# Kernel optimization log

Hardware: AMD Instinct MI355X
Metric: run time of the kernel (lower is better)

The kernel has to match this reference:

```python
import jax, jax.numpy as jnp
import numpy as np

B, N_IN, D_IN, N_OUT, D_OUT, ROUTINGS = 512, 1152, 8, 10, 16, 3


def squash(s, axis=-1):
    # scale = |s|^2 / (1 + |s|^2) / (|s| + 1e-8)
    norm = jnp.linalg.norm(s, axis=axis, keepdims=True)
    return (norm ** 2 / (1.0 + norm ** 2) / (norm + 1e-8)) * s


def setup_inputs() -> dict:
    key = jax.random.key(0)
    k1, k2 = jax.random.split(key)
    x = jax.random.normal(k1, (B, N_IN, D_IN), dtype=jnp.float32)
    weight = 0.01 * jax.random.normal(k2, (N_OUT, N_IN, D_OUT, D_IN), dtype=jnp.float32)
    return {"x": x, "weight": weight}


def reference(x, weight):
    # x: [B, N_IN, D_IN]; weight: [N_OUT, N_IN, D_OUT, D_IN]
    # x_hat[b,o,n,:] = weight[o,n] @ x[b,n]  -> [B, N_OUT, N_IN, D_OUT]
    x_hat = jnp.einsum('onij,bnj->boni', weight, x)
    x_hat_det = jax.lax.stop_gradient(x_hat)

    # routing logits b: [B, N_OUT, N_IN]
    b = jnp.zeros(x_hat.shape[:3], dtype=x_hat.dtype)
    outputs = None
    for i in range(ROUTINGS):
        c = jax.nn.softmax(b, axis=1)  # softmax over output capsules
        if i == ROUTINGS - 1:
            outputs = squash(jnp.sum(c[..., None] * x_hat, axis=2))  # [B, N_OUT, D_OUT]
        else:
            outputs = squash(jnp.sum(c[..., None] * x_hat_det, axis=2))
            # agreement: b += <outputs, x_hat_det> over D_OUT
            b = b + jnp.einsum('bod,bond->bon', outputs, x_hat_det)
    return outputs  # [B, N_OUT, D_OUT]
```

## Files before the change

### kernel.cpp

```cpp
#include <hip/hip_runtime.h>
#include <hip/hip_bf16.h>
#include <hip/hip_fp16.h>

#define B_    512
#define NI    1152
#define NO    10
#define BT    16
#define NBT   32
#define NC    24
#define NCH   48
#define RNDS  6
#define RN    8

typedef __attribute__((ext_vector_type(8))) short bf16x8;
typedef __attribute__((ext_vector_type(4))) float f32x4;
typedef __attribute__((ext_vector_type(8))) unsigned short u16x8;

#define SPART_H    ((size_t)NC * NBT * NO * 256)
#define OUTSUM_F32 ((size_t)NBT * NO * 256)
#define XB_US      ((size_t)NBT * NC * RNDS * 1024)
#define WB_US      ((size_t)NC * RNDS * 12288)

__device__ inline unsigned short f2bf(float f) {
    __hip_bfloat16 h = __float2bfloat16(f);
    return *reinterpret_cast<unsigned short*>(&h);
}

__device__ __forceinline__ bf16x8 load_cvt8(const float* src) {
    f32x4 v0 = *reinterpret_cast<const f32x4*>(src);
    f32x4 v1 = *reinterpret_cast<const f32x4*>(src + 4);
    u16x8 u = { f2bf(v0[0]), f2bf(v0[1]), f2bf(v0[2]), f2bf(v0[3]),
                f2bf(v1[0]), f2bf(v1[1]), f2bf(v1[2]), f2bf(v1[3]) };
    return *reinterpret_cast<bf16x8*>(&u);
}

__device__ __forceinline__ void iter_epilogue(
    uint2 (*red)[NO * 64], const f32x4* sacc, float sc,
    int w, int l, int tid, unsigned short* base)
{
    #pragma unroll
    for (int o = 0; o < NO; ++o) {
        __half2 h01 = __floats2half2_rn(sacc[o][0] * sc, sacc[o][1] * sc);
        __half2 h23 = __floats2half2_rn(sacc[o][2] * sc, sacc[o][3] * sc);
        red[w][o * 64 + l] =
            make_uint2(*reinterpret_cast<unsigned int*>(&h01),
                       *reinterpret_cast<unsigned int*>(&h23));
    }
    __syncthreads();
    for (int g = tid; g < NO * 64; g += 256) {
        uint2 a0 = red[0][g], a1 = red[1][g], a2 = red[2][g], a3 = red[3][g];
        auto h2f2 = [](unsigned int u) {
            __half2 h = *reinterpret_cast<__half2*>(&u);
            return __half22float2(h);
        };
        float2 lo = h2f2(a0.x), l1 = h2f2(a1.x), l2 = h2f2(a2.x), l3 = h2f2(a3.x);
        float2 ho = h2f2(a0.y), h1 = h2f2(a1.y), h2 = h2f2(a2.y), h3 = h2f2(a3.y);
        float2 sl = { (lo.x + l1.x) + (l2.x + l3.x), (lo.y + l1.y) + (l2.y + l3.y) };
        float2 sh = { (ho.x + h1.x) + (h2.x + h3.x), (ho.y + h1.y) + (h2.y + h3.y) };
        __half2 p01 = __floats2half2_rn(sl.x, sl.y);
        __half2 p23 = __floats2half2_rn(sh.x, sh.y);
        *reinterpret_cast<uint2*>(base + (size_t)g * 4) =
            make_uint2(*reinterpret_cast<unsigned int*>(&p01),
                       *reinterpret_cast<unsigned int*>(&p23));
    }
}

__global__ __launch_bounds__(256) void caps_f0(
    const float* __restrict__ x, const float* __restrict__ w,
    unsigned short* __restrict__ xb, unsigned short* __restrict__ wb,
    unsigned short* __restrict__ s_part)
{
    __shared__ uint2 red[4][NO * 64];

    const int tid = threadIdx.x;
    const int wv  = tid >> 6;
    const int l   = tid & 63;
    const int b16 = l & 15;
    const int hi  = l >> 4;
    const int blk = blockIdx.x;
    const int xcd = blk & 7, idx = blk >> 3;
    const int nc  = xcd * 3 + (idx >> 5);
    const int bt  = idx & 31;

    #pragma unroll
    for (int k = 0; k < 3; ++k) {
        const int gid = k * 256 + tid;
        const int r   = gid >> 7, m = gid & 127;
        const int nl  = m >> 4, bl = m & 15;
        const int b   = bt * BT + bl;
        const int n   = nc * NCH + r * RN + nl;
        const size_t img = (size_t)(bt * NC + nc) * RNDS + r;
        bf16x8 u = load_cvt8(x + ((size_t)b * NI + n) * 8);
        *reinterpret_cast<bf16x8*>(xb + (img * 128 + m) * 8) = u;
    }

    #pragma unroll
    for (int k = 0; k < 2; ++k) {
        const int loc = k * 256 + tid;
        if (loc < 288) {
            const int t    = blk * 288 + loc;
            const int lane = t & 63;
            const int gs   = (t >> 6) % 24;
            const int img  = t / 1536;
            const int h2   = lane >> 4, d = lane & 15;
            const int nl   = gs / 3, oq = gs % 3;
            const int r    = img % RNDS, ncw = img / RNDS;
            const int o    = oq * 4 + h2;
            const int n    = ncw * NCH + r * RN + nl;
            bf16x8 u = (bf16x8){0,0,0,0,0,0,0,0};
            if (o < NO)
                u = load_cvt8(w + ((size_t)o * NI + n) * 128 + d * 8);
            *reinterpret_cast<bf16x8*>(wb + (size_t)t * 8) = u;
        }
    }

    f32x4 sacc[NO];
    #pragma unroll
    for (int o = 0; o < NO; ++o) sacc[o] = (f32x4){0.f, 0.f, 0.f, 0.f};

    const int bg = bt * BT + b16;
    #pragma unroll 1
    for (int g = 0; g < 3; ++g) {
        const int n_lane = nc * NCH + wv * 12 + g * 4 + hi;
        bf16x8 bv4 = load_cvt8(x + ((size_t)bg * NI + n_lane) * 8);
        #pragma unroll
        for (int o = 0; o < NO; ++o) {
            bf16x8 av4 = load_cvt8(w + ((size_t)o * NI + n_lane) * 128 + b16 * 8);
            sacc[o] = __builtin_amdgcn_mfma_f32_16x16x32_bf16(
                av4, bv4, sacc[o], 0, 0, 0);
        }
    }

    iter_epilogue(red, sacc, 0.1f, wv, l, tid,
                  s_part + ((size_t)nc * NBT + bt) * 2560);
}

__global__ __launch_bounds__(256, 3) void caps_itr(
    const unsigned short* __restrict__ xb,
    const unsigned short* __restrict__ wb,
    const float* __restrict__ outsum,
    unsigned short* __restrict__ s_part)
{
    __shared__ uint2 red[4][NO * 64];

    const int tid = threadIdx.x;
    const int wv  = tid >> 6;
    const int l   = tid & 63;
    const int b16 = l & 15;
    const int hi  = l >> 4;
    const int blk = blockIdx.x;
    const int xcd = blk & 7, idx = blk >> 3;
    const int nc  = xcd * 3 + (idx >> 5);
    const int bt  = idx & 31;

    f32x4 outf[NO];
    #pragma unroll
    for (int o = 0; o < NO; ++o)
        outf[o] = *reinterpret_cast<const f32x4*>(
            outsum + (((size_t)bt * NO + o) * 64 + l) * 4);

    f32x4 sacc[NO];
    #pragma unroll
    for (int o = 0; o < NO; ++o) sacc[o] = (f32x4){0.f, 0.f, 0.f, 0.f};

    const unsigned short* xbase = xb + (size_t)(bt * NC + nc) * (RNDS * 1024);
    const unsigned short* wbase = wb + (size_t)nc * (RNDS * 12288);

    #pragma unroll 1
    for (int r = 0; r < RNDS; ++r) {
        const unsigned short* xr = xbase + (size_t)r * 1024;
        const unsigned short* wr = wbase + (size_t)r * 12288;
        #pragma unroll 1
        for (int i = 0; i < 2; ++i) {
            const int nl = wv * 2 + i;
            bf16x8 bv = *reinterpret_cast<const bf16x8*>(
                xr + nl * 128 + b16 * 8);
            bf16x8 avv[3];
            #pragma unroll
            for (int oq = 0; oq < 3; ++oq)
                avv[oq] = *reinterpret_cast<const bf16x8*>(
                    wr + (nl * 3 + oq) * 512 + l * 8);
            bf16x8 bvt[4];
            #pragma unroll
            for (int t = 0; t < 4; ++t)
                bvt[t] = (hi == t) ? bv : (bf16x8){0,0,0,0,0,0,0,0};

            f32x4 xh[NO];
            float lg[NO];
            #pragma unroll
            for (int oq = 0; oq < 3; ++oq) {
                const int tmax = (oq < 2) ? 4 : 2;
                #pragma unroll
                for (int t = 0; t < tmax; ++t) {
                    const int o = oq * 4 + t;
                    xh[o] = __builtin_amdgcn_mfma_f32_16x16x32_bf16(
                        avv[oq], bvt[t], (f32x4){0.f, 0.f, 0.f, 0.f}, 0, 0, 0);
                    float pp = outf[o][0] * xh[o][0];
                    pp = fmaf(outf[o][1], xh[o][1], pp);
                    pp = fmaf(outf[o][2], xh[o][2], pp);
                    pp = fmaf(outf[o][3], xh[o][3], pp);
                    pp += __shfl_xor(pp, 16, 64);
                    pp += __shfl_xor(pp, 32, 64);
                    lg[o] = pp;
                }
            }
            float sum = 0.f;
            #pragma unroll
            for (int o = 0; o < NO; ++o) { lg[o] = __expf(lg[o]); sum += lg[o]; }
            const float rs = __builtin_amdgcn_rcpf(sum);
            #pragma unroll
            for (int o = 0; o < NO; ++o) {
                const float cc = lg[o] * rs;
                sacc[o][0] = fmaf(cc, xh[o][0], sacc[o][0]);
                sacc[o][1] = fmaf(cc, xh[o][1], sacc[o][1]);
                sacc[o][2] = fmaf(cc, xh[o][2], sacc[o][2]);
                sacc[o][3] = fmaf(cc, xh[o][3], sacc[o][3]);
            }
        }
    }

    iter_epilogue(red, sacc, 1.0f, wv, l, tid,
                  s_part + ((size_t)nc * NBT + bt) * 2560);
}

template<int MODE>
__global__ __launch_bounds__(256) void caps_squash(
    const unsigned short* __restrict__ s_part,
    float* __restrict__ outsum,
    float* __restrict__ dout)
{
    __shared__ float sq[256];
    const int bo = blockIdx.x;
    const int t  = threadIdx.x;

    float s = 0.f;
    #pragma unroll 4
    for (int nc = 0; nc < NC; ++nc) {
        __half h = *reinterpret_cast<const __half*>(
            s_part + ((size_t)nc * NBT * NO + bo) * 256 + t);
        s += __half2float(h);
    }

    float n2 = s * s;
    n2 += __shfl_xor(n2, 1, 64);
    n2 += __shfl_xor(n2, 2, 64);
    sq[t] = n2;
    __syncthreads();
    const int base = t & 63;
    n2 = (sq[base] + sq[64 + base]) + (sq[128 + base] + sq[192 + base]);

    const float norm  = sqrtf(n2);
    const float scale = n2 / ((1.f + n2) * (norm + 1e-8f));
    const float v = scale * s;

    if constexpr (MODE == 0) {
        outsum[(size_t)bo * 256 + t] = v;
    } else if constexpr (MODE == 1) {
        outsum[(size_t)bo * 256 + t] += v;
    } else {
        const int bt = bo / NO, o = bo - bt * NO;
        const int b16 = (t >> 2) & 15, hi = t >> 6, q = t & 3;
        dout[((size_t)(bt * BT + b16) * NO + o) * 16 + hi * 4 + q] = v;
    }
}

extern "C" void kernel_launch(void* const* d_in, const int* in_sizes, int n_in,
                              void* d_out, int out_size, void* d_ws, size_t ws_size,
                              hipStream_t stream) {
    const float* x = (const float*)d_in[0];
    const float* w = (const float*)d_in[1];
    float* out = (float*)d_out;

    unsigned short* s_part = (unsigned short*)d_ws;
    float*          outsum = (float*)(s_part + SPART_H);
    unsigned short* xb     = (unsigned short*)(outsum + OUTSUM_F32);
    unsigned short* wb     = xb + XB_US;

    dim3 gI(NBT * NC), bI(256);
    dim3 gS(NBT * NO), bS(256);

    caps_f0<<<gI, bI, 0, stream>>>(x, w, xb, wb, s_part);
    caps_squash<0><<<gS, bS, 0, stream>>>(s_part, outsum, nullptr);
    caps_itr<<<gI, bI, 0, stream>>>(xb, wb, outsum, s_part);
    caps_squash<1><<<gS, bS, 0, stream>>>(s_part, outsum, nullptr);
    caps_itr<<<gI, bI, 0, stream>>>(xb, wb, outsum, s_part);
    caps_squash<2><<<gS, bS, 0, stream>>>(s_part, nullptr, out);
}
```

Measured before the change: 68.27 us.

## Fuse intermediate squash reductions into routing iteration kernel prologue

The two intermediate caps_squash launches are removed. Each caps_itr block now reduces the fp16 partial sums across all chunks itself, applies squash, and builds its agreement vectors directly. The s_part buffer is double-buffered so one iteration can read the previous partials while writing new ones. Only the first iteration writes outsum; the second adds the stored value in registers. This saves two kernel launches and their dependency gaps, but every one of the 24 chunk blocks per batch tile now repeats the same cross-chunk reduction, which adds a lot of redundant L2 traffic and serial latency before the MFMA loop starts.

Result: slower. 109.1 us (+59.8%).

```diff
diff --git a/kernel.cpp b/kernel.cpp
--- a/kernel.cpp
+++ b/kernel.cpp
@@ -135,11 +135,13 @@
                   s_part + ((size_t)nc * NBT + bt) * 2560);
 }
 
+template<int IT>
 __global__ __launch_bounds__(256, 3) void caps_itr(
     const unsigned short* __restrict__ xb,
     const unsigned short* __restrict__ wb,
-    const float* __restrict__ outsum,
-    unsigned short* __restrict__ s_part)
+    const unsigned short* __restrict__ s_prev,
+    float* __restrict__ outsum,
+    unsigned short* __restrict__ s_next)
 {
     __shared__ uint2 red[4][NO * 64];
 
@@ -155,9 +157,33 @@
 
     f32x4 outf[NO];
     #pragma unroll
-    for (int o = 0; o < NO; ++o)
-        outf[o] = *reinterpret_cast<const f32x4*>(
-            outsum + (((size_t)bt * NO + o) * 64 + l) * 4);
+    for (int o = 0; o < NO; ++o) {
+        f32x4 s = (f32x4){0.f, 0.f, 0.f, 0.f};
+        #pragma unroll 6
+        for (int c = 0; c < NC; ++c) {
+            uint2 pk = *reinterpret_cast<const uint2*>(
+                s_prev + ((((size_t)c * NBT + bt) * NO + o) * 64 + l) * 4);
+            __half2 h01 = *reinterpret_cast<__half2*>(&pk.x);
+            __half2 h23 = *reinterpret_cast<__half2*>(&pk.y);
+            float2 f01 = __half22float2(h01), f23 = __half22float2(h23);
+            s[0] += f01.x; s[1] += f01.y; s[2] += f23.x; s[3] += f23.y;
+        }
+        float n2 = s[0] * s[0] + s[1] * s[1] + s[2] * s[2] + s[3] * s[3];
+        n2 += __shfl_xor(n2, 16, 64);
+        n2 += __shfl_xor(n2, 32, 64);
+        const float norm  = sqrtf(n2);
+        const float scale = n2 / ((1.f + n2) * (norm + 1e-8f));
+        f32x4 v = { scale * s[0], scale * s[1], scale * s[2], scale * s[3] };
+        if constexpr (IT == 1) {
+            *reinterpret_cast<f32x4*>(
+                outsum + (((size_t)bt * NO + o) * 64 + l) * 4) = v;
+            outf[o] = v;
+        } else {
+            f32x4 p = *reinterpret_cast<const f32x4*>(
+                outsum + (((size_t)bt * NO + o) * 64 + l) * 4);
+            outf[o] = (f32x4){p[0] + v[0], p[1] + v[1], p[2] + v[2], p[3] + v[3]};
+        }
+    }
 
     f32x4 sacc[NO];
     #pragma unroll
@@ -220,13 +246,11 @@
     }
 
     iter_epilogue(red, sacc, 1.0f, wv, l, tid,
-                  s_part + ((size_t)nc * NBT + bt) * 2560);
-}
-
-template<int MODE>
-__global__ __launch_bounds__(256) void caps_squash(
+                  s_next + ((size_t)nc * NBT + bt) * 2560);
+}
+
+__global__ __launch_bounds__(256) void caps_squash_final(
     const unsigned short* __restrict__ s_part,
-    float* __restrict__ outsum,
     float* __restrict__ dout)
 {
     __shared__ float sq[256];
@@ -253,15 +277,9 @@
     const float scale = n2 / ((1.f + n2) * (norm + 1e-8f));
     const float v = scale * s;
 
-    if constexpr (MODE == 0) {
-        outsum[(size_t)bo * 256 + t] = v;
-    } else if constexpr (MODE == 1) {
-        outsum[(size_t)bo * 256 + t] += v;
-    } else {
-        const int bt = bo / NO, o = bo - bt * NO;
-        const int b16 = (t >> 2) & 15, hi = t >> 6, q = t & 3;
-        dout[((size_t)(bt * BT + b16) * NO + o) * 16 + hi * 4 + q] = v;
-    }
+    const int bt = bo / NO, o = bo - bt * NO;
+    const int b16 = (t >> 2) & 15, hi = t >> 6, q = t & 3;
+    dout[((size_t)(bt * BT + b16) * NO + o) * 16 + hi * 4 + q] = v;
 }
 
 extern "C" void kernel_launch(void* const* d_in, const int* in_sizes, int n_in,
@@ -271,18 +289,17 @@
     const float* w = (const float*)d_in[1];
     float* out = (float*)d_out;
 
-    unsigned short* s_part = (unsigned short*)d_ws;
-    float*          outsum = (float*)(s_part + SPART_H);
-    unsigned short* xb     = (unsigned short*)(outsum + OUTSUM_F32);
-    unsigned short* wb     = xb + XB_US;
+    unsigned short* s_partA = (unsigned short*)d_ws;
+    unsigned short* s_partB = s_partA + SPART_H;
+    float*          outsum  = (float*)(s_partB + SPART_H);
+    unsigned short* xb      = (unsigned short*)(outsum + OUTSUM_F32);
+    unsigned short* wb      = xb + XB_US;
 
     dim3 gI(NBT * NC), bI(256);
     dim3 gS(NBT * NO), bS(256);
 
-    caps_f0<<<gI, bI, 0, stream>>>(x, w, xb, wb, s_part);
-    caps_squash<0><<<gS, bS, 0, stream>>>(s_part, outsum, nullptr);
-    caps_itr<<<gI, bI, 0, stream>>>(xb, wb, outsum, s_part);
-    caps_squash<1><<<gS, bS, 0, stream>>>(s_part, outsum, nullptr);
-    caps_itr<<<gI, bI, 0, stream>>>(xb, wb, outsum, s_part);
-    caps_squash<2><<<gS, bS, 0, stream>>>(s_part, nullptr, out);
-}
+    caps_f0<<<gI, bI, 0, stream>>>(x, w, xb, wb, s_partA);
+    caps_itr<1><<<gI, bI, 0, stream>>>(xb, wb, s_partA, outsum, s_partB);
+    caps_itr<2><<<gI, bI, 0, stream>>>(xb, wb, s_partB, outsum, s_partA);
+    caps_squash_final<<<gS, bS, 0, stream>>>(s_partA, out);
+}
```

## Split fp32-to-bf16 conversion into a separate kernel and read pre-converted operands in first pass

Applied to the files above, without the earlier changes.

The first routing pass used to convert x and weight to bf16 inline while also re-reading and converting the weight from fp32 for its own MFMAs. A dedicated conversion kernel now writes bf16 x, the existing weight layout, and a new MFMA-ready weight layout (wb2). The first iteration kernel then reads bf16 operands directly. This cuts redundant fp32 weight reads and conversion work, but adds an extra launch, extra workspace, and a write plus read-back of wb2.

Measured after the change: 65.86 us, median of 2. 1.04x faster.

```diff
diff --git a/kernel.cpp b/kernel.cpp
--- a/kernel.cpp
+++ b/kernel.cpp
@@ -20,6 +20,7 @@
 #define OUTSUM_F32 ((size_t)NBT * NO * 256)
 #define XB_US      ((size_t)NBT * NC * RNDS * 1024)
 #define WB_US      ((size_t)NC * RNDS * 12288)
+#define WB2_US     ((size_t)NC * 12 * NO * 512)
 
 __device__ inline unsigned short f2bf(float f) {
     __hip_bfloat16 h = __float2bfloat16(f);
@@ -65,9 +66,50 @@
     }
 }
 
-__global__ __launch_bounds__(256) void caps_f0(
+__global__ __launch_bounds__(256) void cvt_xw(
     const float* __restrict__ x, const float* __restrict__ w,
     unsigned short* __restrict__ xb, unsigned short* __restrict__ wb,
+    unsigned short* __restrict__ wb2)
+{
+    const int blk = blockIdx.x;
+    if (blk < 2304) {
+        const int t = blk * 256 + threadIdx.x;
+        const int m   = t & 127;
+        const int img = t >> 7;
+        const int nl  = m >> 4, bl = m & 15;
+        const int r   = img % RNDS;
+        const int bc  = img / RNDS;
+        const int nc  = bc % NC, bt = bc / NC;
+        const int b   = bt * BT + bl;
+        const int n   = nc * NCH + r * RN + nl;
+        bf16x8 u = load_cvt8(x + ((size_t)b * NI + n) * 8);
+        *reinterpret_cast<bf16x8*>(xb + (size_t)t * 8) = u;
+    } else {
+        const int t    = (blk - 2304) * 256 + threadIdx.x;
+        const int lane = t & 63;
+        const int gs   = (t >> 6) % 24;
+        const int img  = t / 1536;
+        const int h2   = lane >> 4, d = lane & 15;
+        const int nl   = gs / 3, oq = gs % 3;
+        const int r    = img % RNDS, nc = img / RNDS;
+        const int o    = oq * 4 + h2;
+        const int n    = nc * NCH + r * RN + nl;
+        bf16x8 u = (bf16x8){0,0,0,0,0,0,0,0};
+        if (o < NO) {
+            u = load_cvt8(w + ((size_t)o * NI + n) * 128 + d * 8);
+            const int g2  = r * 2 + (nl >> 2);
+            const int hi2 = nl & 3;
+            *reinterpret_cast<bf16x8*>(
+                wb2 + (((size_t)nc * 12 + g2) * NO + o) * 512
+                    + (hi2 * 16 + d) * 8) = u;
+        }
+        *reinterpret_cast<bf16x8*>(wb + (size_t)t * 8) = u;
+    }
+}
+
+__global__ __launch_bounds__(256) void caps_it0(
+    const unsigned short* __restrict__ xb,
+    const unsigned short* __restrict__ wb2,
     unsigned short* __restrict__ s_part)
 {
     __shared__ uint2 red[4][NO * 64];
@@ -82,50 +124,24 @@
     const int nc  = xcd * 3 + (idx >> 5);
     const int bt  = idx & 31;
 
-    #pragma unroll
-    for (int k = 0; k < 3; ++k) {
-        const int gid = k * 256 + tid;
-        const int r   = gid >> 7, m = gid & 127;
-        const int nl  = m >> 4, bl = m & 15;
-        const int b   = bt * BT + bl;
-        const int n   = nc * NCH + r * RN + nl;
-        const size_t img = (size_t)(bt * NC + nc) * RNDS + r;
-        bf16x8 u = load_cvt8(x + ((size_t)b * NI + n) * 8);
-        *reinterpret_cast<bf16x8*>(xb + (img * 128 + m) * 8) = u;
-    }
-
-    #pragma unroll
-    for (int k = 0; k < 2; ++k) {
-        const int loc = k * 256 + tid;
-        if (loc < 288) {
-            const int t    = blk * 288 + loc;
-            const int lane = t & 63;
-            const int gs   = (t >> 6) % 24;
-            const int img  = t / 1536;
-            const int h2   = lane >> 4, d = lane & 15;
-            const int nl   = gs / 3, oq = gs % 3;
-            const int r    = img % RNDS, ncw = img / RNDS;
-            const int o    = oq * 4 + h2;
-            const int n    = ncw * NCH + r * RN + nl;
-            bf16x8 u = (bf16x8){0,0,0,0,0,0,0,0};
-            if (o < NO)
-                u = load_cvt8(w + ((size_t)o * NI + n) * 128 + d * 8);
-            *reinterpret_cast<bf16x8*>(wb + (size_t)t * 8) = u;
-        }
-    }
-
     f32x4 sacc[NO];
     #pragma unroll
     for (int o = 0; o < NO; ++o) sacc[o] = (f32x4){0.f, 0.f, 0.f, 0.f};
 
-    const int bg = bt * BT + b16;
+    const unsigned short* xbase = xb + (size_t)(bt * NC + nc) * (RNDS * 1024);
+    const unsigned short* w2base = wb2 + (size_t)nc * (12 * NO * 512);
+
     #pragma unroll 1
-    for (int g = 0; g < 3; ++g) {
-        const int n_lane = nc * NCH + wv * 12 + g * 4 + hi;
-        bf16x8 bv4 = load_cvt8(x + ((size_t)bg * NI + n_lane) * 8);
+    for (int gi = 0; gi < 3; ++gi) {
+        const int g  = wv * 3 + gi;
+        const int nn = 4 * g + hi;
+        const int r  = nn >> 3, nl = nn & 7;
+        bf16x8 bv4 = *reinterpret_cast<const bf16x8*>(
+            xbase + (size_t)r * 1024 + (nl * 16 + b16) * 8);
         #pragma unroll
         for (int o = 0; o < NO; ++o) {
-            bf16x8 av4 = load_cvt8(w + ((size_t)o * NI + n_lane) * 128 + b16 * 8);
+            bf16x8 av4 = *reinterpret_cast<const bf16x8*>(
+                w2base + ((size_t)g * NO + o) * 512 + l * 8);
             sacc[o] = __builtin_amdgcn_mfma_f32_16x16x32_bf16(
                 av4, bv4, sacc[o], 0, 0, 0);
         }
@@ -275,11 +291,13 @@
     float*          outsum = (float*)(s_part + SPART_H);
     unsigned short* xb     = (unsigned short*)(outsum + OUTSUM_F32);
     unsigned short* wb     = xb + XB_US;
+    unsigned short* wb2    = wb + WB_US;
 
     dim3 gI(NBT * NC), bI(256);
     dim3 gS(NBT * NO), bS(256);
 
-    caps_f0<<<gI, bI, 0, stream>>>(x, w, xb, wb, s_part);
+    cvt_xw<<<dim3(3168), dim3(256), 0, stream>>>(x, w, xb, wb, wb2);
+    caps_it0<<<gI, bI, 0, stream>>>(xb, wb2, s_part);
     caps_squash<0><<<gS, bS, 0, stream>>>(s_part, outsum, nullptr);
     caps_itr<<<gI, bI, 0, stream>>>(xb, wb, outsum, s_part);
     caps_squash<1><<<gS, bS, 0, stream>>>(s_part, outsum, nullptr);
```
